# Kernel tuning notes

Measured on AMD Instinct MI355X. Metric: run time of the kernel, lower is better.

The kernel has to match this reference:

```python
import jax, jax.numpy as jnp
import numpy as np

N_NODES = 50000
N_EDGES = 1_600_000
IN_F = 128
OUT_F = 32
HEADS = 4
EDGE_F = 4
EDGE_HID = 32


def setup_inputs() -> dict:
    key = jax.random.key(0)
    ks = jax.random.split(key, 12)
    x = jax.random.normal(ks[0], (N_NODES, IN_F), dtype=jnp.float32)
    edge_index = jax.random.randint(ks[1], (2, N_EDGES), 0, N_NODES, dtype=jnp.int32)
    edge_attr = jax.random.normal(ks[2], (N_EDGES, EDGE_F), dtype=jnp.float32)
    # linear: in_features -> heads*out_features (stored as [in, out] for x @ W)
    W = jax.random.normal(ks[3], (IN_F, HEADS * OUT_F), dtype=jnp.float32) * (1.0 / np.sqrt(IN_F))
    b = jnp.zeros((HEADS * OUT_F,), dtype=jnp.float32)
    # edge_proj: Linear(EDGE_F,32) -> ReLU -> Linear(32, heads)
    eW1 = jax.random.normal(ks[4], (EDGE_F, EDGE_HID), dtype=jnp.float32) * (1.0 / np.sqrt(EDGE_F))
    eb1 = jnp.zeros((EDGE_HID,), dtype=jnp.float32)
    eW2 = jax.random.normal(ks[5], (EDGE_HID, HEADS), dtype=jnp.float32) * (1.0 / np.sqrt(EDGE_HID))
    eb2 = jnp.zeros((HEADS,), dtype=jnp.float32)
    att_src = jax.random.normal(ks[6], (1, HEADS, OUT_F), dtype=jnp.float32) * 0.1
    att_dst = jax.random.normal(ks[7], (1, HEADS, OUT_F), dtype=jnp.float32) * 0.1
    return {"x": x, "edge_index": edge_index, "edge_attr": edge_attr,
            "W": W, "b": b, "eW1": eW1, "eb1": eb1, "eW2": eW2, "eb2": eb2,
            "att_src": att_src, "att_dst": att_dst}


def reference(x, edge_index, edge_attr, W, b, eW1, eb1, eW2, eb2, att_src, att_dst):
    N = x.shape[0]
    src, dst = edge_index[0], edge_index[1]
    E = src.shape[0]

    h = (x @ W + b).reshape(N, HEADS, OUT_F)                     # [N,H,F]
    alpha_src = jnp.sum(h[src] * att_src, axis=-1)               # [E,H]
    alpha_dst = jnp.sum(h[dst] * att_dst, axis=-1)               # [E,H]
    edge_att = jax.nn.relu(edge_attr @ eW1 + eb1) @ eW2 + eb2    # [E,H]
    alpha = jax.nn.leaky_relu(alpha_src + alpha_dst + edge_att, negative_slope=0.2)

    # softmax_by_src: dense [N,H] buffer of -inf, scatter-set by src
    # softmax over the NODE axis, then gather back per edge.
    last = jax.ops.segment_max(jnp.arange(E, dtype=jnp.int32), src, num_segments=N)  # [N]
    valid = last >= 0
    dense = jnp.where(valid[:, None], alpha[jnp.clip(last, 0)], -jnp.inf)  # [N,H]
    dense = jax.nn.softmax(dense, axis=0)
    alpha_e = dense[src]                                         # [E,H]

    # dropout: module default training=False path (identity), eval mode
    # scatter-add aggregation: out[src] += h[dst] * alpha_e (all heads at once)
    msg = h[dst] * alpha_e[:, :, None]                           # [E,H,F]
    out = jnp.zeros_like(h).at[src].add(msg)                     # [N,H,F]
    return out.mean(axis=1)                                      # [N,F]
```

## Files before the change

kernel.cpp:

```cpp
#include <hip/hip_runtime.h>
#include <hip/hip_fp16.h>
#include <math.h>


#define SUPCAP 9216
#define AGG_CAP 2048
#define BIN_CHUNK 2048

__global__ __launch_bounds__(256, 4) void k_pre(
    const float* __restrict__ x, const float* __restrict__ W,
    const float* __restrict__ b, const float* __restrict__ att_src,
    const float* __restrict__ att_dst, __half* __restrict__ hbuf16,
    float* __restrict__ s_, float* __restrict__ t_,
    const int* __restrict__ src, const int* __restrict__ dst,
    int* __restrict__ bcur, unsigned* __restrict__ bin_y,
    unsigned* __restrict__ bin_e,
    int N, int E, int nsup, int ngemm, int nbin) {
  __shared__ __align__(16) float smem[8448];
  int tx = threadIdx.x;
  int bid = blockIdx.x;
  int mmin = (nbin < ngemm) ? nbin : ngemm;
  int m2 = 2 * mmin;
  bool isbin;
  int wid;
  if (bid < m2) { isbin = (bid & 1); wid = bid >> 1; }
  else { isbin = (nbin > ngemm); wid = mmin + (bid - m2); }

  if (isbin) {
    uint2* ebuf = (uint2*)smem;
    int* hist = (int*)(smem + 4096);
    int* bas  = hist + 256;
    int* curs = bas + 256;
    int* gpos = curs + 256;
    int e0 = wid * BIN_CHUNK;
    int n = E - e0; if (n > BIN_CHUNK) n = BIN_CHUNK;
    hist[tx] = 0;
    __syncthreads();
    for (int i = tx; i < n; i += 256) {
      atomicAdd(&hist[src[e0 + i] >> 8], 1);
    }
    __syncthreads();
    int v = hist[tx];
    bas[tx] = v;
    __syncthreads();
    for (int off = 1; off < 256; off <<= 1) {
      int t = (tx >= off) ? bas[tx - off] : 0;
      __syncthreads();
      bas[tx] += t;
      __syncthreads();
    }
    curs[tx] = bas[tx] - v;
    if (tx < nsup && v > 0) gpos[tx] = atomicAdd(&bcur[tx], v);
    __syncthreads();
    for (int i = tx; i < n; i += 256) {
      int e = e0 + i;
      int s = src[e], d = dst[e];
      int pos = atomicAdd(&curs[s >> 8], 1);
      unsigned loc = (unsigned)(s & 255);
      ebuf[pos] = make_uint2((loc << 24) | (unsigned)e, (loc << 16) | (unsigned)d);
    }
    __syncthreads();
    int wave = tx >> 6, lane = tx & 63;
    for (int bb = wave; bb < nsup; bb += 4) {
      int cnt = hist[bb];
      if (cnt == 0) continue;
      int lbase = bas[bb] - cnt;
      int g = gpos[bb];
      unsigned* dpy = bin_y + (size_t)bb * SUPCAP + g;
      unsigned* dpe = bin_e + (size_t)bb * SUPCAP + g;
      for (int i = lane; i < cnt; i += 64)
        if (g + i < SUPCAP) {
          uint2 w = ebuf[lbase + i];
          dpe[i] = w.x;
          dpy[i] = w.y;
        }
    }
  } else {
    float* xs = smem;
    float* ws = smem + 32 * 132;
    int r0 = wid * 32;
    const float4* xg = (const float4*)(x + (size_t)r0 * 128);
#pragma unroll
    for (int j = 0; j < 4; ++j) {
      int l = tx + j * 256;
      int row = l >> 5, col4 = l & 31;
      float4 v = make_float4(0.f, 0.f, 0.f, 0.f);
      if (r0 + row < N) v = xg[l];
      *(float4*)(xs + row * 132 + col4 * 4) = v;
    }
    int cg = tx & 15, rg = tx >> 4;
    float acc[2][8];
#pragma unroll
    for (int r = 0; r < 2; ++r)
#pragma unroll
      for (int c = 0; c < 8; ++c) acc[r][c] = 0.f;
    const float4* Wg4 = (const float4*)W;
    const float* xbase = xs + rg * 2 * 132;
    int woff = cg * 8 + ((cg >> 3) << 2);
    for (int kt = 0; kt < 4; ++kt) {
      __syncthreads();
#pragma unroll
      for (int j = 0; j < 4; ++j) {
        int ll = tx + j * 256;
        int row = ll >> 5, c4 = ll & 31;
        *(float4*)(ws + row * 132 + c4 * 4 + ((c4 >> 4) << 2)) = Wg4[kt * 1024 + ll];
      }
      __syncthreads();
#pragma unroll 2
      for (int k4 = 0; k4 < 8; ++k4) {
        float4 xr0 = *(const float4*)(xbase + kt * 32 + k4 * 4);
        float4 xr1 = *(const float4*)(xbase + 132 + kt * 32 + k4 * 4);
#pragma unroll
        for (int kk = 0; kk < 4; ++kk) {
          const float* wrow = ws + (k4 * 4 + kk) * 132 + woff;
          float4 w0 = *(const float4*)(wrow);
          float4 w1 = *(const float4*)(wrow + 4);
          const float wc[8] = {w0.x, w0.y, w0.z, w0.w, w1.x, w1.y, w1.z, w1.w};
          float xv0 = ((const float*)&xr0)[kk];
          float xv1 = ((const float*)&xr1)[kk];
#pragma unroll
          for (int c = 0; c < 8; ++c) {
            acc[0][c] += xv0 * wc[c];
            acc[1][c] += xv1 * wc[c];
          }
        }
      }
    }
    float4 b0 = ((const float4*)b)[cg * 2],       b1 = ((const float4*)b)[cg * 2 + 1];
    float4 s0 = ((const float4*)att_src)[cg * 2], s1 = ((const float4*)att_src)[cg * 2 + 1];
    float4 d0 = ((const float4*)att_dst)[cg * 2], d1 = ((const float4*)att_dst)[cg * 2 + 1];
    const float bbv[8] = {b0.x, b0.y, b0.z, b0.w, b1.x, b1.y, b1.z, b1.w};
    const float asv[8] = {s0.x, s0.y, s0.z, s0.w, s1.x, s1.y, s1.z, s1.w};
    const float adv[8] = {d0.x, d0.y, d0.z, d0.w, d1.x, d1.y, d1.z, d1.w};
    int hd = cg >> 2;
#pragma unroll
    for (int r = 0; r < 2; ++r) {
      float o[8];
#pragma unroll
      for (int c = 0; c < 8; ++c) o[c] = acc[r][c] + bbv[c];
      float sp = 0.f, tp = 0.f;
#pragma unroll
      for (int c = 0; c < 8; ++c) { sp += o[c] * asv[c]; tp += o[c] * adv[c]; }
      sp += __shfl_xor(sp, 1); sp += __shfl_xor(sp, 2);
      tp += __shfl_xor(tp, 1); tp += __shfl_xor(tp, 2);
      int grow = r0 + rg * 2 + r;
      if (grow < N) {
        __half2 h0 = __floats2half2_rn(o[0], o[1]);
        __half2 h1 = __floats2half2_rn(o[2], o[3]);
        __half2 h2 = __floats2half2_rn(o[4], o[5]);
        __half2 h3 = __floats2half2_rn(o[6], o[7]);
        uint4 u;
        u.x = *(unsigned*)&h0; u.y = *(unsigned*)&h1;
        u.z = *(unsigned*)&h2; u.w = *(unsigned*)&h3;
        ((uint4*)(hbuf16 + (size_t)grow * 128))[cg] = u;
        if ((tx & 3) == 0) {
          s_[grow * 4 + hd] = sp;
          t_[grow * 4 + hd] = tp;
        }
      }
    }
  }
}

__global__ __launch_bounds__(256) void k_dense(
    const int* __restrict__ bcur, const unsigned* __restrict__ bin_e,
    const unsigned* __restrict__ bin_y,
    const int* __restrict__ dst, const float* __restrict__ edge_attr,
    const float* __restrict__ eW1, const float* __restrict__ eb1,
    const float* __restrict__ eW2, const float* __restrict__ eb2,
    const float* __restrict__ s_, const float* __restrict__ t_,
    float* __restrict__ dense, float* __restrict__ pmax,
    float* __restrict__ psum,
    unsigned short* __restrict__ sorted_dst,
    int* __restrict__ noff, int* __restrict__ ncnt, int N) {
  __shared__ int lastv[256];
  __shared__ int hist[256], bas[256], curs[256];
  __shared__ float lm[256 * 4], ls[256 * 4];
  int sp = blockIdx.x, tx = threadIdx.x;
  lastv[tx] = -1;
  hist[tx] = 0;
  __syncthreads();
  int cnt = bcur[sp]; if (cnt > SUPCAP) cnt = SUPCAP;
  const unsigned* be = bin_e + (size_t)sp * SUPCAP;
  const unsigned* by = bin_y + (size_t)sp * SUPCAP;
  for (int i = tx; i < cnt; i += 256) {
    unsigned p = be[i];
    atomicMax(&lastv[p >> 24], (int)(p & 0xFFFFFF));
    atomicAdd(&hist[by[i] >> 16], 1);
  }
  __syncthreads();
  int v = hist[tx];
  bas[tx] = v;
  __syncthreads();
  for (int off = 1; off < 256; off <<= 1) {
    int t = (tx >= off) ? bas[tx - off] : 0;
    __syncthreads();
    bas[tx] += t;
    __syncthreads();
  }
  curs[tx] = bas[tx] - v;
  int gn = sp * 256 + tx;
  noff[gn] = sp * SUPCAP + bas[tx] - v;
  ncnt[gn] = v;
  __syncthreads();
  unsigned short* sd = sorted_dst + (size_t)sp * SUPCAP;
  for (int i = tx; i < cnt; i += 256) {
    unsigned y = by[i];
    int pos = atomicAdd(&curs[y >> 16], 1);
    sd[pos] = (unsigned short)y;
  }
  float vv[4] = {-INFINITY, -INFINITY, -INFINITY, -INFINITY};
  if (gn < N) {
    int e = lastv[tx];
    if (e >= 0) {
      int d = dst[e];
      const float* ea = edge_attr + (size_t)e * 4;
      float e0 = ea[0], e1 = ea[1], e2 = ea[2], e3 = ea[3];
      float a0 = eb2[0], a1 = eb2[1], a2 = eb2[2], a3 = eb2[3];
#pragma unroll
      for (int i = 0; i < 32; ++i) {
        float hid = eb1[i] + e0 * eW1[i] + e1 * eW1[32 + i] + e2 * eW1[64 + i] + e3 * eW1[96 + i];
        hid = fmaxf(hid, 0.f);
        a0 += hid * eW2[i * 4 + 0]; a1 += hid * eW2[i * 4 + 1];
        a2 += hid * eW2[i * 4 + 2]; a3 += hid * eW2[i * 4 + 3];
      }
      float w0 = s_[gn * 4 + 0] + t_[d * 4 + 0] + a0;
      float w1 = s_[gn * 4 + 1] + t_[d * 4 + 1] + a1;
      float w2 = s_[gn * 4 + 2] + t_[d * 4 + 2] + a2;
      float w3 = s_[gn * 4 + 3] + t_[d * 4 + 3] + a3;
      vv[0] = w0 > 0.f ? w0 : 0.2f * w0;
      vv[1] = w1 > 0.f ? w1 : 0.2f * w1;
      vv[2] = w2 > 0.f ? w2 : 0.2f * w2;
      vv[3] = w3 > 0.f ? w3 : 0.2f * w3;
    }
#pragma unroll
    for (int h = 0; h < 4; ++h) dense[gn * 4 + h] = vv[h];
  }
#pragma unroll
  for (int h = 0; h < 4; ++h) {
    lm[tx * 4 + h] = vv[h];
    ls[tx * 4 + h] = (vv[h] > -INFINITY) ? 1.f : 0.f;
  }
  __syncthreads();
  for (int off = 128; off > 0; off >>= 1) {
    if (tx < off) {
#pragma unroll
      for (int h = 0; h < 4; ++h) {
        float m2 = lm[(tx + off) * 4 + h], s2 = ls[(tx + off) * 4 + h];
        float m1 = lm[tx * 4 + h], s1 = ls[tx * 4 + h];
        float M = fmaxf(m1, m2);
        if (M > -INFINITY) {
          ls[tx * 4 + h] = s1 * expf(m1 - M) + s2 * expf(m2 - M);
          lm[tx * 4 + h] = M;
        }
      }
    }
    __syncthreads();
  }
  if (tx == 0) {
#pragma unroll
    for (int h = 0; h < 4; ++h) {
      pmax[sp * 4 + h] = lm[h];
      psum[sp * 4 + h] = ls[h];
    }
  }
}

__global__ void k_smax2(const float* __restrict__ pmax, const float* __restrict__ psum,
                        int nb, float* __restrict__ gmax, float* __restrict__ ginv) {
  int tx = threadIdx.x;
  int h = tx & 3, chunk = tx >> 2;
  float m = -INFINITY, s = 0.f;
  for (int bq = chunk; bq < nb; bq += 64) {
    float m2 = pmax[bq * 4 + h], s2 = psum[bq * 4 + h];
    float M = fmaxf(m, m2);
    if (M > -INFINITY) {
      s = s * expf(m - M) + s2 * expf(m2 - M);
      m = M;
    }
  }
  __shared__ float lm[256], ls[256];
  lm[tx] = m; ls[tx] = s;
  __syncthreads();
  for (int off = 128; off >= 4; off >>= 1) {
    if (tx < off) {
      float m2 = lm[tx + off], s2 = ls[tx + off];
      float m1 = lm[tx], s1 = ls[tx];
      float M = fmaxf(m1, m2);
      if (M > -INFINITY) {
        ls[tx] = s1 * expf(m1 - M) + s2 * expf(m2 - M);
        lm[tx] = M;
      }
    }
    __syncthreads();
  }
  if (tx < 4) {
    gmax[tx] = lm[tx];
    ginv[tx] = 1.f / ls[tx];
  }
}

#define ACC(r, P, Q) { \
  float2 f0 = __half22float2(*(__half2*)&r.x), f1 = __half22float2(*(__half2*)&r.y); \
  float2 f2 = __half22float2(*(__half2*)&r.z), f3 = __half22float2(*(__half2*)&r.w); \
  P.x += f0.x; P.y += f0.y; P.z += f1.x; P.w += f1.y; \
  Q.x += f2.x; Q.y += f2.y; Q.z += f3.x; Q.w += f3.y; }

__global__ __launch_bounds__(256) void k_agg(
    const unsigned short* __restrict__ sorted_dst,
    const int* __restrict__ noff, const int* __restrict__ ncnt,
    const __half* __restrict__ hbuf16, const float* __restrict__ dense,
    const float* __restrict__ gmax, const float* __restrict__ ginv,
    float* __restrict__ out, int N) {
  __shared__ unsigned short sl[AGG_CAP];
  int tx = threadIdx.x;
  int n0 = blockIdx.x << 4;
  int nlast = n0 + 15; if (nlast > N - 1) nlast = N - 1;
  int lstart = noff[n0];
  int lend = noff[nlast] + ncnt[nlast];
  int total = lend - lstart; if (total > AGG_CAP) total = AGG_CAP;
  for (int i = tx; i < total; i += 256) sl[i] = sorted_dst[lstart + i];
  __syncthreads();
  int g = tx >> 4, l = tx & 15;
  int n = n0 + g;
  if (n >= N) return;
  int beg = noff[n] - lstart;
  int cnt = ncnt[n];
  if (beg + cnt > total) cnt = total - beg;
  int end = beg + cnt;
  int hd = l >> 2;
  float w = expf(dense[(size_t)n * 4 + hd] - gmax[hd]) * ginv[hd];
  float4 p0 = {0, 0, 0, 0}, q0 = {0, 0, 0, 0};
  float4 p1 = {0, 0, 0, 0}, q1 = {0, 0, 0, 0};
  int e = beg;
  for (; e + 7 < end; e += 8) {
    int c0 = sl[e],     c1 = sl[e + 1], c2 = sl[e + 2], c3 = sl[e + 3];
    int c4_ = sl[e + 4], c5 = sl[e + 5], c6 = sl[e + 6], c7 = sl[e + 7];
    uint4 r0 = *((const uint4*)(hbuf16 + ((size_t)c0  << 7)) + l);
    uint4 r1 = *((const uint4*)(hbuf16 + ((size_t)c1  << 7)) + l);
    uint4 r2 = *((const uint4*)(hbuf16 + ((size_t)c2  << 7)) + l);
    uint4 r3 = *((const uint4*)(hbuf16 + ((size_t)c3  << 7)) + l);
    uint4 r4 = *((const uint4*)(hbuf16 + ((size_t)c4_ << 7)) + l);
    uint4 r5 = *((const uint4*)(hbuf16 + ((size_t)c5  << 7)) + l);
    uint4 r6 = *((const uint4*)(hbuf16 + ((size_t)c6  << 7)) + l);
    uint4 r7 = *((const uint4*)(hbuf16 + ((size_t)c7  << 7)) + l);
    ACC(r0, p0, q0); ACC(r1, p1, q1); ACC(r2, p0, q0); ACC(r3, p1, q1);
    ACC(r4, p0, q0); ACC(r5, p1, q1); ACC(r6, p0, q0); ACC(r7, p1, q1);
  }
  for (; e + 3 < end; e += 4) {
    int c0 = sl[e], c1 = sl[e + 1], c2 = sl[e + 2], c3 = sl[e + 3];
    uint4 r0 = *((const uint4*)(hbuf16 + ((size_t)c0 << 7)) + l);
    uint4 r1 = *((const uint4*)(hbuf16 + ((size_t)c1 << 7)) + l);
    uint4 r2 = *((const uint4*)(hbuf16 + ((size_t)c2 << 7)) + l);
    uint4 r3 = *((const uint4*)(hbuf16 + ((size_t)c3 << 7)) + l);
    ACC(r0, p0, q0); ACC(r1, p1, q1); ACC(r2, p0, q0); ACC(r3, p1, q1);
  }
  for (; e < end; ++e) {
    int c0 = sl[e];
    uint4 r0 = *((const uint4*)(hbuf16 + ((size_t)c0 << 7)) + l);
    ACC(r0, p0, q0);
  }
  p0.x += p1.x; p0.y += p1.y; p0.z += p1.z; p0.w += p1.w;
  q0.x += q1.x; q0.y += q1.y; q0.z += q1.z; q0.w += q1.w;
  p0.x *= w; p0.y *= w; p0.z *= w; p0.w *= w;
  q0.x *= w; q0.y *= w; q0.z *= w; q0.w *= w;
  p0.x += __shfl_xor(p0.x, 4);  p0.y += __shfl_xor(p0.y, 4);
  p0.z += __shfl_xor(p0.z, 4);  p0.w += __shfl_xor(p0.w, 4);
  q0.x += __shfl_xor(q0.x, 4);  q0.y += __shfl_xor(q0.y, 4);
  q0.z += __shfl_xor(q0.z, 4);  q0.w += __shfl_xor(q0.w, 4);
  p0.x += __shfl_xor(p0.x, 8);  p0.y += __shfl_xor(p0.y, 8);
  p0.z += __shfl_xor(p0.z, 8);  p0.w += __shfl_xor(p0.w, 8);
  q0.x += __shfl_xor(q0.x, 8);  q0.y += __shfl_xor(q0.y, 8);
  q0.z += __shfl_xor(q0.z, 8);  q0.w += __shfl_xor(q0.w, 8);
  if (l < 4) {
    float4 oA, oB;
    oA.x = 0.25f * p0.x; oA.y = 0.25f * p0.y; oA.z = 0.25f * p0.z; oA.w = 0.25f * p0.w;
    oB.x = 0.25f * q0.x; oB.y = 0.25f * q0.y; oB.z = 0.25f * q0.z; oB.w = 0.25f * q0.w;
    *(float4*)(out + (size_t)n * 32 + l * 8) = oA;
    *(float4*)(out + (size_t)n * 32 + l * 8 + 4) = oB;
  }
}

extern "C" void kernel_launch(void* const* d_in, const int* in_sizes, int n_in,
                              void* d_out, int out_size, void* d_ws, size_t ws_size,
                              hipStream_t stream) {
  const float* x        = (const float*)d_in[0];
  const int*   ei       = (const int*)d_in[1];
  const float* edge_attr= (const float*)d_in[2];
  const float* W        = (const float*)d_in[3];
  const float* b        = (const float*)d_in[4];
  const float* eW1      = (const float*)d_in[5];
  const float* eb1      = (const float*)d_in[6];
  const float* eW2      = (const float*)d_in[7];
  const float* eb2      = (const float*)d_in[8];
  const float* att_src  = (const float*)d_in[9];
  const float* att_dst  = (const float*)d_in[10];
  float* out = (float*)d_out;

  const int N = in_sizes[0] / 128;
  const int E = in_sizes[1] / 2;
  const int* src = ei;
  const int* dst = ei + E;
  const int NSUP = (N + 255) >> 8;

  char* wp = (char*)d_ws;
  auto alloc = [&](size_t bytes) -> void* {
    void* p = (void*)wp;
    wp += (bytes + 255) & ~(size_t)255;
    return p;
  };
  __half* hbuf16 = (__half*)alloc((size_t)N * 128 * 2);
  float* s_    = (float*)alloc((size_t)N * 4 * 4);
  float* t_    = (float*)alloc((size_t)N * 4 * 4);
  float* dense = (float*)alloc((size_t)N * 4 * 4);
  float* pmax  = (float*)alloc((size_t)NSUP * 4 * 4);
  float* psum  = (float*)alloc((size_t)NSUP * 4 * 4);
  float* gmax  = (float*)alloc(4 * 4);
  float* ginv  = (float*)alloc(4 * 4);
  int* bcur    = (int*)alloc((size_t)NSUP * 4);
  unsigned* bin_y = (unsigned*)alloc((size_t)NSUP * SUPCAP * 4);
  unsigned* bin_e = (unsigned*)alloc((size_t)NSUP * SUPCAP * 4);
  unsigned short* sorted_dst = (unsigned short*)alloc((size_t)NSUP * SUPCAP * 2);
  int* noff    = (int*)alloc((size_t)NSUP * 256 * 4);
  int* ncnt    = (int*)alloc((size_t)NSUP * 256 * 4);

  const int NGEMM = (N + 31) / 32;
  const int NBIN  = (E + BIN_CHUNK - 1) / BIN_CHUNK;

  hipMemsetAsync(bcur, 0, (size_t)NSUP * 4, stream);
  k_pre<<<NGEMM + NBIN, 256, 0, stream>>>(x, W, b, att_src, att_dst, hbuf16, s_, t_,
                                          src, dst, bcur, bin_y, bin_e,
                                          N, E, NSUP, NGEMM, NBIN);
  k_dense<<<NSUP, 256, 0, stream>>>(bcur, bin_e, bin_y, dst, edge_attr, eW1, eb1, eW2, eb2,
                                    s_, t_, dense, pmax, psum, sorted_dst, noff, ncnt, N);
  k_smax2<<<1, 256, 0, stream>>>(pmax, psum, NSUP, gmax, ginv);
  k_agg<<<(N + 15) / 16, 256, 0, stream>>>(sorted_dst, noff, ncnt, hbuf16, dense, gmax, ginv, out, N);
}
```

Baseline: 243.7 us.

## Fuse softmax reduce into aggregation, enlarge GEMM tile, flatten bin scatter

The single-block global softmax reduction kernel is removed. Every aggregation block now recomputes the max and sum over the per-superbin partials itself, which saves one launch at the cost of redundant work in each of roughly 3k blocks. The GEMM path now processes 64 rows per block with a 4x8 register tile, which raises shared memory and register use and lowers the occupancy hint to 3. The bin write-out loop now assigns one element per thread and finds its bin by binary search over the prefix sums, instead of having each wave walk whole bins.

```diff
diff --git a/kernel.cpp b/kernel.cpp
--- a/kernel.cpp
+++ b/kernel.cpp
@@ -7,7 +7,7 @@
 #define AGG_CAP 2048
 #define BIN_CHUNK 2048
 
-__global__ __launch_bounds__(256, 4) void k_pre(
+__global__ __launch_bounds__(256, 3) void k_pre(
     const float* __restrict__ x, const float* __restrict__ W,
     const float* __restrict__ b, const float* __restrict__ att_src,
     const float* __restrict__ att_dst, __half* __restrict__ hbuf16,
@@ -16,7 +16,7 @@
     int* __restrict__ bcur, unsigned* __restrict__ bin_y,
     unsigned* __restrict__ bin_e,
     int N, int E, int nsup, int ngemm, int nbin) {
-  __shared__ __align__(16) float smem[8448];
+  __shared__ __align__(16) float smem[12672];
   int tx = threadIdx.x;
   int bid = blockIdx.x;
   int mmin = (nbin < ngemm) ? nbin : ngemm;
@@ -60,28 +60,28 @@
       ebuf[pos] = make_uint2((loc << 24) | (unsigned)e, (loc << 16) | (unsigned)d);
     }
     __syncthreads();
-    int wave = tx >> 6, lane = tx & 63;
-    for (int bb = wave; bb < nsup; bb += 4) {
-      int cnt = hist[bb];
-      if (cnt == 0) continue;
-      int lbase = bas[bb] - cnt;
-      int g = gpos[bb];
-      unsigned* dpy = bin_y + (size_t)bb * SUPCAP + g;
-      unsigned* dpe = bin_e + (size_t)bb * SUPCAP + g;
-      for (int i = lane; i < cnt; i += 64)
-        if (g + i < SUPCAP) {
-          uint2 w = ebuf[lbase + i];
-          dpe[i] = w.x;
-          dpy[i] = w.y;
-        }
+    for (int i = tx; i < n; i += 256) {
+      uint2 w = ebuf[i];
+      int lo = 0, hi = 255;
+      while (lo < hi) {
+        int mid = (lo + hi) >> 1;
+        if (bas[mid] > i) hi = mid; else lo = mid + 1;
+      }
+      int bb = lo;
+      int lbase = bas[bb] - hist[bb];
+      int off = gpos[bb] + (i - lbase);
+      if (off < SUPCAP) {
+        bin_e[(size_t)bb * SUPCAP + off] = w.x;
+        bin_y[(size_t)bb * SUPCAP + off] = w.y;
+      }
     }
   } else {
     float* xs = smem;
-    float* ws = smem + 32 * 132;
-    int r0 = wid * 32;
+    float* ws = smem + 64 * 132;
+    int r0 = wid * 64;
     const float4* xg = (const float4*)(x + (size_t)r0 * 128);
 #pragma unroll
-    for (int j = 0; j < 4; ++j) {
+    for (int j = 0; j < 8; ++j) {
       int l = tx + j * 256;
       int row = l >> 5, col4 = l & 31;
       float4 v = make_float4(0.f, 0.f, 0.f, 0.f);
@@ -89,13 +89,13 @@
       *(float4*)(xs + row * 132 + col4 * 4) = v;
     }
     int cg = tx & 15, rg = tx >> 4;
-    float acc[2][8];
-#pragma unroll
-    for (int r = 0; r < 2; ++r)
+    float acc[4][8];
+#pragma unroll
+    for (int r = 0; r < 4; ++r)
 #pragma unroll
       for (int c = 0; c < 8; ++c) acc[r][c] = 0.f;
     const float4* Wg4 = (const float4*)W;
-    const float* xbase = xs + rg * 2 * 132;
+    const float* xbase = xs + rg * 4 * 132;
     int woff = cg * 8 + ((cg >> 3) << 2);
     for (int kt = 0; kt < 4; ++kt) {
       __syncthreads();
@@ -110,6 +110,8 @@
       for (int k4 = 0; k4 < 8; ++k4) {
         float4 xr0 = *(const float4*)(xbase + kt * 32 + k4 * 4);
         float4 xr1 = *(const float4*)(xbase + 132 + kt * 32 + k4 * 4);
+        float4 xr2 = *(const float4*)(xbase + 264 + kt * 32 + k4 * 4);
+        float4 xr3 = *(const float4*)(xbase + 396 + kt * 32 + k4 * 4);
 #pragma unroll
         for (int kk = 0; kk < 4; ++kk) {
           const float* wrow = ws + (k4 * 4 + kk) * 132 + woff;
@@ -118,10 +120,14 @@
           const float wc[8] = {w0.x, w0.y, w0.z, w0.w, w1.x, w1.y, w1.z, w1.w};
           float xv0 = ((const float*)&xr0)[kk];
           float xv1 = ((const float*)&xr1)[kk];
+          float xv2 = ((const float*)&xr2)[kk];
+          float xv3 = ((const float*)&xr3)[kk];
 #pragma unroll
           for (int c = 0; c < 8; ++c) {
             acc[0][c] += xv0 * wc[c];
             acc[1][c] += xv1 * wc[c];
+            acc[2][c] += xv2 * wc[c];
+            acc[3][c] += xv3 * wc[c];
           }
         }
       }
@@ -134,7 +140,7 @@
     const float adv[8] = {d0.x, d0.y, d0.z, d0.w, d1.x, d1.y, d1.z, d1.w};
     int hd = cg >> 2;
 #pragma unroll
-    for (int r = 0; r < 2; ++r) {
+    for (int r = 0; r < 4; ++r) {
       float o[8];
 #pragma unroll
       for (int c = 0; c < 8; ++c) o[c] = acc[r][c] + bbv[c];
@@ -143,7 +149,7 @@
       for (int c = 0; c < 8; ++c) { sp += o[c] * asv[c]; tp += o[c] * adv[c]; }
       sp += __shfl_xor(sp, 1); sp += __shfl_xor(sp, 2);
       tp += __shfl_xor(tp, 1); tp += __shfl_xor(tp, 2);
-      int grow = r0 + rg * 2 + r;
+      int grow = r0 + rg * 4 + r;
       if (grow < N) {
         __half2 h0 = __floats2half2_rn(o[0], o[1]);
         __half2 h1 = __floats2half2_rn(o[2], o[3]);
@@ -266,40 +272,6 @@
   }
 }
 
-__global__ void k_smax2(const float* __restrict__ pmax, const float* __restrict__ psum,
-                        int nb, float* __restrict__ gmax, float* __restrict__ ginv) {
-  int tx = threadIdx.x;
-  int h = tx & 3, chunk = tx >> 2;
-  float m = -INFINITY, s = 0.f;
-  for (int bq = chunk; bq < nb; bq += 64) {
-    float m2 = pmax[bq * 4 + h], s2 = psum[bq * 4 + h];
-    float M = fmaxf(m, m2);
-    if (M > -INFINITY) {
-      s = s * expf(m - M) + s2 * expf(m2 - M);
-      m = M;
-    }
-  }
-  __shared__ float lm[256], ls[256];
-  lm[tx] = m; ls[tx] = s;
-  __syncthreads();
-  for (int off = 128; off >= 4; off >>= 1) {
-    if (tx < off) {
-      float m2 = lm[tx + off], s2 = ls[tx + off];
-      float m1 = lm[tx], s1 = ls[tx];
-      float M = fmaxf(m1, m2);
-      if (M > -INFINITY) {
-        ls[tx] = s1 * expf(m1 - M) + s2 * expf(m2 - M);
-        lm[tx] = M;
-      }
-    }
-    __syncthreads();
-  }
-  if (tx < 4) {
-    gmax[tx] = lm[tx];
-    ginv[tx] = 1.f / ls[tx];
-  }
-}
-
 #define ACC(r, P, Q) { \
   float2 f0 = __half22float2(*(__half2*)&r.x), f1 = __half22float2(*(__half2*)&r.y); \
   float2 f2 = __half22float2(*(__half2*)&r.z), f3 = __half22float2(*(__half2*)&r.w); \
@@ -310,9 +282,11 @@
     const unsigned short* __restrict__ sorted_dst,
     const int* __restrict__ noff, const int* __restrict__ ncnt,
     const __half* __restrict__ hbuf16, const float* __restrict__ dense,
-    const float* __restrict__ gmax, const float* __restrict__ ginv,
+    const float* __restrict__ pmax, const float* __restrict__ psum, int nb,
     float* __restrict__ out, int N) {
   __shared__ unsigned short sl[AGG_CAP];
+  __shared__ float lm[256], ls[256];
+  __shared__ float sgm[4], sgi[4];
   int tx = threadIdx.x;
   int n0 = blockIdx.x << 4;
   int nlast = n0 + 15; if (nlast > N - 1) nlast = N - 1;
@@ -320,7 +294,37 @@
   int lend = noff[nlast] + ncnt[nlast];
   int total = lend - lstart; if (total > AGG_CAP) total = AGG_CAP;
   for (int i = tx; i < total; i += 256) sl[i] = sorted_dst[lstart + i];
-  __syncthreads();
+  {
+    int h = tx & 3, chunk = tx >> 2;
+    float m = -INFINITY, s = 0.f;
+    for (int bq = chunk; bq < nb; bq += 64) {
+      float m2 = pmax[bq * 4 + h], s2 = psum[bq * 4 + h];
+      float M = fmaxf(m, m2);
+      if (M > -INFINITY) {
+        s = s * expf(m - M) + s2 * expf(m2 - M);
+        m = M;
+      }
+    }
+    lm[tx] = m; ls[tx] = s;
+    __syncthreads();
+    for (int off = 128; off >= 4; off >>= 1) {
+      if (tx < off) {
+        float m2 = lm[tx + off], s2 = ls[tx + off];
+        float m1 = lm[tx], s1 = ls[tx];
+        float M = fmaxf(m1, m2);
+        if (M > -INFINITY) {
+          ls[tx] = s1 * expf(m1 - M) + s2 * expf(m2 - M);
+          lm[tx] = M;
+        }
+      }
+      __syncthreads();
+    }
+    if (tx < 4) {
+      sgm[tx] = lm[tx];
+      sgi[tx] = 1.f / ls[tx];
+    }
+    __syncthreads();
+  }
   int g = tx >> 4, l = tx & 15;
   int n = n0 + g;
   if (n >= N) return;
@@ -329,7 +333,7 @@
   if (beg + cnt > total) cnt = total - beg;
   int end = beg + cnt;
   int hd = l >> 2;
-  float w = expf(dense[(size_t)n * 4 + hd] - gmax[hd]) * ginv[hd];
+  float w = expf(dense[(size_t)n * 4 + hd] - sgm[hd]) * sgi[hd];
   float4 p0 = {0, 0, 0, 0}, q0 = {0, 0, 0, 0};
   float4 p1 = {0, 0, 0, 0}, q1 = {0, 0, 0, 0};
   int e = beg;
@@ -415,8 +419,6 @@
   float* dense = (float*)alloc((size_t)N * 4 * 4);
   float* pmax  = (float*)alloc((size_t)NSUP * 4 * 4);
   float* psum  = (float*)alloc((size_t)NSUP * 4 * 4);
-  float* gmax  = (float*)alloc(4 * 4);
-  float* ginv  = (float*)alloc(4 * 4);
   int* bcur    = (int*)alloc((size_t)NSUP * 4);
   unsigned* bin_y = (unsigned*)alloc((size_t)NSUP * SUPCAP * 4);
   unsigned* bin_e = (unsigned*)alloc((size_t)NSUP * SUPCAP * 4);
@@ -424,7 +426,7 @@
   int* noff    = (int*)alloc((size_t)NSUP * 256 * 4);
   int* ncnt    = (int*)alloc((size_t)NSUP * 256 * 4);
 
-  const int NGEMM = (N + 31) / 32;
+  const int NGEMM = (N + 63) / 64;
   const int NBIN  = (E + BIN_CHUNK - 1) / BIN_CHUNK;
 
   hipMemsetAsync(bcur, 0, (size_t)NSUP * 4, stream);
@@ -433,6 +435,6 @@
                                           N, E, NSUP, NGEMM, NBIN);
   k_dense<<<NSUP, 256, 0, stream>>>(bcur, bin_e, bin_y, dst, edge_attr, eW1, eb1, eW2, eb2,
                                     s_, t_, dense, pmax, psum, sorted_dst, noff, ncnt, N);
-  k_smax2<<<1, 256, 0, stream>>>(pmax, psum, NSUP, gmax, ginv);
-  k_agg<<<(N + 15) / 16, 256, 0, stream>>>(sorted_dst, noff, ncnt, hbuf16, dense, gmax, ginv, out, N);
+  k_agg<<<(N + 15) / 16, 256, 0, stream>>>(sorted_dst, noff, ncnt, hbuf16, dense,
+                                           pmax, psum, NSUP, out, N);
 }
```

Result: no change. 239.3 us (median of 2 runs) (-1.8%).
